# Performance work log

Measured on AMD Instinct MI355X. Metric: run time of the kernel, lower is better.

The kernel has to match this reference:

```python
import jax, jax.numpy as jnp
import numpy as np

B, T, IN = 256, 512, 4      # batch, seq_len, input dim
M, D, NS = 3, 256, 64       # n kaarma models, dictionary size, state dim
H = 128                     # controller (GRU) hidden size
GU, GS = 0.5, 0.5           # gaussian kernel widths (input / state)


def setup_inputs() -> dict:
    key = jax.random.key(0)
    ks = jax.random.split(key, 12)
    s = lambda k, shp, sc: (jax.random.normal(k, shp, dtype=jnp.float32) * sc)
    return {
        "x": s(ks[0], (B, T, IN), 1.0),
        "y": s(ks[1], (B, T), 1.0),
        # MKAARMA: per-model dictionary (inputs U, states S) and coefficients A
        "U": s(ks[2], (M, D, IN), 1.0),
        "S": s(ks[3], (M, D, NS), 0.3),
        "A": s(ks[4], (M, D, NS), 1.0 / np.sqrt(D)),
        # GRU controller (input dim = M + 1 error channel)
        "W_ih": s(ks[5], (M + 1, 3 * H), 1.0 / np.sqrt(M + 1)),
        "W_hh": s(ks[6], (H, 3 * H), 1.0 / np.sqrt(H)),
        "b_ih": s(ks[7], (3 * H,), 0.1),
        "b_hh": s(ks[8], (3 * H,), 0.1),
        # linear_decode: (H-1) -> M gate logits
        "Wd": s(ks[9], (H - 1, M), 1.0 / np.sqrt(H - 1)),
        "bd": s(ks[10], (M,), 0.1),
    }


def _forward(x, y, U, S, A, W_ih, W_hh, b_ih, b_hh, Wd, bd):
    init_gate = jnp.array([[0.3333, 0.3333, 0.3334]], dtype=x.dtype)

    def step(carry, xs):
        s, h, gate_prev, err = carry          # [B,NS], [B,H], [B,M], [B]
        x_t, y_t = xs                         # [B,IN], [B]
        # --- mkaarma: gaussian input*state kernel against dictionary ---
        du = jnp.sum((x_t[:, None, None, :] - U[None]) ** 2, axis=-1)  # [B,M,D]
        ds = jnp.sum((s[:, None, None, :] - S[None]) ** 2, axis=-1)   # [B,M,D]
        K = jnp.exp(-GU * du - GS * ds)                                # [B,M,D]
        new_state = jnp.einsum('bmd,mdn->bmn', K, A)                   # [B,M,NS]
        encoded = jnp.max(K, axis=-1)                                  # [B,M]
        # --- controller: GRU cell on [similarities, error] ---
        inp = jnp.concatenate([encoded, err[:, None]], axis=1)         # [B,M+1]
        gi = inp @ W_ih + b_ih
        gh = h @ W_hh + b_hh
        ir, iz, inn = jnp.split(gi, 3, axis=1)
        hr, hz, hn = jnp.split(gh, 3, axis=1)
        r = jax.nn.sigmoid(ir + hr)
        z = jax.nn.sigmoid(iz + hz)
        n = jnp.tanh(inn + r * hn)
        h_new = (1.0 - z) * n + z * h                                  # [B,H]
        # --- gate decode + theta blend ---
        gate = jax.nn.softmax(h_new[:, :-1] @ Wd + bd, axis=1)          # [B,M]
        theta = jax.nn.sigmoid(h_new[:, -1:])                           # [B,1]
        gate = gate * theta + gate_prev * (1.0 - theta)
        s_new = jnp.einsum('bm,bmn->bn', gate, new_state)               # [B,NS]
        pred = s_new[:, -1]                                             # [B]
        err_new = pred - y_t
        penalty = jnp.sum(gate * (1.0 - gate), axis=1, keepdims=True)   # [B,1]
        return (s_new, h_new, gate, err_new), (pred, penalty)

    carry0 = (
        jnp.zeros((x.shape[0], NS), x.dtype),
        jnp.zeros((x.shape[0], H), x.dtype),
        jnp.tile(init_gate, (x.shape[0], 1)),
        jnp.ones((x.shape[0],), x.dtype),
    )
    xs = (jnp.swapaxes(x, 0, 1), jnp.swapaxes(y, 0, 1))  # time-major
    _, (o, p) = jax.lax.scan(step, carry0, xs)
    return jnp.swapaxes(o, 0, 1), jnp.swapaxes(p, 0, 1)   # [B,T], [B,T,1]


def reference(x, y, U, S, A, W_ih, W_hh, b_ih, b_hh, Wd, bd):
    return _forward(x, y, U, S, A, W_ih, W_hh, b_ih, b_hh, Wd, bd)
```

## Files before the change

kernel.cpp:

```cpp
#include <hip/hip_runtime.h>
#include <math.h>

constexpr int kB  = 256;
constexpr int kT  = 512;
constexpr int kNS = 64;
constexpr int kH  = 128;

constexpr int kWRowsLds = 256;
constexpr int kWPad     = 132;

__device__ __forceinline__ float sigmoidf_(float v) { return 1.0f / (1.0f + __expf(-v)); }
__device__ __forceinline__ float dot4(float4 a, float4 b) {
    return a.x*b.x + a.y*b.y + a.z*b.z + a.w*b.w;
}

extern "C" __global__ void __launch_bounds__(256)
whh_transpose(const float* __restrict__ Whh, float* __restrict__ WhhT) {
    const int o = blockIdx.x * 256 + threadIdx.x;
    const int j = o >> 7, k = o & 127;
    WhhT[o] = Whh[k * 384 + j];
}

extern "C" __global__ void __launch_bounds__(512, 2)
disc_kernel(const float* __restrict__ x,   const float* __restrict__ y,
            const float* __restrict__ U,   const float* __restrict__ S,
            const float* __restrict__ A,   const float* __restrict__ Wih,
            const float* __restrict__ bih, const float* __restrict__ bhh,
            const float* __restrict__ Wd,  const float* __restrict__ bd,
            const float* __restrict__ WhhT,
            float* __restrict__ out_o,  float* __restrict__ out_p)
{
    const int b    = blockIdx.x;
    const int tid  = threadIdx.x;
    const int lane = tid & 63;
    const int wid  = tid >> 6;
    const int hb   = tid & 1;

    __shared__ __align__(16) float sh_K[768];
    __shared__ __align__(16) float sh_part[512];
    __shared__ __align__(16) float sh_part2[512];
    __shared__ __align__(16) float sh_gh[384];
    __shared__ __align__(16) float sh_h[2][kH];
    __shared__ __align__(16) float sh_s[kNS];
    __shared__ __align__(16) float sh_Wih[4 * 384];
    __shared__ __align__(16) float sh_bih[384];
    __shared__ __align__(16) float sh_bhh[384];
    __shared__ float sh_Wd[384];
    __shared__ float sh_bd[4];
    __shared__ float sh_encA[8];
    __shared__ float sh_encB[8];
    __shared__ __align__(16) float sh_xt[4];
    __shared__ float sh_x2, sh_s2, sh_err;
    __shared__ float sh_yt[2];
    __shared__ __align__(16) float sh_W[kWRowsLds * kWPad];

    const float4* S4 = reinterpret_cast<const float4*>(S);
    const float4* U4 = reinterpret_cast<const float4*>(U);

    float4 Sa[16]; float4 Ua; float Ca;
    float4 Sb[8];  float Ub0, Ub1; float Cb;
    {
        float ss = 0.f;
#pragma unroll
        for (int j = 0; j < 16; ++j) { Sa[j] = S4[tid * 16 + j]; ss += dot4(Sa[j], Sa[j]); }
        Ua = U4[tid];
        Ca = -0.5f * (dot4(Ua, Ua) + ss);
    }
    const int pbrow = 512 + (tid >> 1);
    {
        float ss = 0.f;
#pragma unroll
        for (int j = 0; j < 8; ++j) { Sb[j] = S4[pbrow * 16 + hb * 8 + j]; ss += dot4(Sb[j], Sb[j]); }
        Ub0 = U[pbrow * 4 + hb * 2 + 0];
        Ub1 = U[pbrow * 4 + hb * 2 + 1];
        Cb = -0.5f * (Ub0*Ub0 + Ub1*Ub1 + ss);
    }
    float A1[64];
#pragma unroll
    for (int dd = 0; dd < 64; ++dd)
        A1[dd] = A[((wid >> 2) * 256 + (wid & 3) * 64 + dd) * 64 + lane];
    float A2[32];
#pragma unroll
    for (int dd = 0; dd < 32; ++dd)
        A2[dd] = A[(512 + (wid >> 1) * 64 + (wid & 1) * 32 + dd) * 64 + lane];

    float g0 = 0.3333f, g1 = 0.3333f, g2 = 0.3334f;

    for (int i = tid; i < 1536; i += 512) sh_Wih[i] = Wih[i];
    for (int i = tid; i < 384; i += 512) {
        sh_bih[i] = bih[i];
        sh_bhh[i] = bhh[i];
        sh_gh[i]  = bhh[i];
        sh_Wd[i]  = (i < 381) ? Wd[i] : 0.f;
    }
    for (int i4 = tid; i4 < kWRowsLds * 32; i4 += 512) {
        const int r = i4 >> 5, c4 = i4 & 31;
        reinterpret_cast<float4*>(sh_W + r * kWPad)[c4] =
            reinterpret_cast<const float4*>(WhhT)[i4];
    }
    if (tid < 3) sh_bd[tid] = bd[tid];
    if (tid < kNS) sh_s[tid] = 0.f;
    if (tid < kH)  sh_h[0][tid] = 0.f;
    if (tid == 0) {
        sh_err = 1.0f; sh_s2 = 0.f;
        float4 xv = reinterpret_cast<const float4*>(x)[(size_t)b * kT];
        reinterpret_cast<float4*>(sh_xt)[0] = xv;
        sh_x2 = dot4(xv, xv);
        sh_yt[0] = y[(size_t)b * kT];
    }
    __syncthreads();

    for (int t = 0; t < kT; ++t) {
        const int par  = t & 1;
        const int par1 = (t + 1) & 1;

        {
            const float scal = -0.5f * (sh_x2 + sh_s2);
            const float4 xt4 = reinterpret_cast<const float4*>(sh_xt)[0];
            const float4* s4 = reinterpret_cast<const float4*>(sh_s);
            float da0 = 0.f, da1 = 0.f, dblo = 0.f, dbhi = 0.f;
#pragma unroll
            for (int j = 0; j < 8; ++j) {
                const float4 sv0 = s4[j];
                const float4 sv1 = s4[8 + j];
                da0  += dot4(sv0, Sa[j]);
                da1  += dot4(sv1, Sa[8 + j]);
                dblo += dot4(sv0, Sb[j]);
                dbhi += dot4(sv1, Sb[j]);
            }
            const float db = hb ? dbhi : dblo;
            const float kk_a = __expf(scal + Ca + dot4(xt4, Ua) + da0 + da1);
            const float xbp  = hb ? (xt4.z*Ub0 + xt4.w*Ub1) : (xt4.x*Ub0 + xt4.y*Ub1);
            const float ph   = db + Cb + xbp;
            const float po   = __shfl_xor(ph, 1, 64);
            const float kk_b = __expf(scal + ph + po);
            sh_K[tid] = kk_a;
            if (hb == 0) sh_K[512 + (tid >> 1)] = kk_b;
            float mA = kk_a, mB = kk_b;
#pragma unroll
            for (int o = 32; o > 0; o >>= 1) {
                mA = fmaxf(mA, __shfl_xor(mA, o, 64));
                mB = fmaxf(mB, __shfl_xor(mB, o, 64));
            }
            if (lane == 0) { sh_encA[wid] = mA; sh_encB[wid] = mB; }
        }
        __syncthreads();

        {
            const float4* K4 = reinterpret_cast<const float4*>(sh_K + wid * 64);
            float acc = 0.f;
#pragma unroll
            for (int j = 0; j < 16; ++j) {
                const float4 kv = K4[j];
                acc += kv.x*A1[4*j] + kv.y*A1[4*j+1] + kv.z*A1[4*j+2] + kv.w*A1[4*j+3];
            }
            sh_part[tid] = acc;
            const float4* K4b = reinterpret_cast<const float4*>(
                                    sh_K + 512 + (wid >> 1) * 64 + (wid & 1) * 32);
            float accb = 0.f;
#pragma unroll
            for (int j = 0; j < 8; ++j) {
                const float4 kv = K4b[j];
                accb += kv.x*A2[4*j] + kv.y*A2[4*j+1] + kv.z*A2[4*j+2] + kv.w*A2[4*j+3];
            }
            sh_part2[tid] = accb;
        }
        if (tid < 128) {
            const float e0 = fmaxf(fmaxf(sh_encA[0], sh_encA[1]), fmaxf(sh_encA[2], sh_encA[3]));
            const float e1 = fmaxf(fmaxf(sh_encA[4], sh_encA[5]), fmaxf(sh_encA[6], sh_encA[7]));
            const float e2 = fmaxf(fmaxf(fmaxf(sh_encB[0], sh_encB[1]), fmaxf(sh_encB[2], sh_encB[3])),
                                   fmaxf(fmaxf(sh_encB[4], sh_encB[5]), fmaxf(sh_encB[6], sh_encB[7])));
            const float er = sh_err;
            const int j = tid;
            const float gir = sh_bih[j]       + e0*sh_Wih[j]        + e1*sh_Wih[384 + j]
                                              + e2*sh_Wih[768 + j]  + er*sh_Wih[1152 + j];
            const float giz = sh_bih[128 + j] + e0*sh_Wih[128 + j]  + e1*sh_Wih[512 + j]
                                              + e2*sh_Wih[896 + j]  + er*sh_Wih[1280 + j];
            const float gin = sh_bih[256 + j] + e0*sh_Wih[256 + j]  + e1*sh_Wih[640 + j]
                                              + e2*sh_Wih[1024 + j] + er*sh_Wih[1408 + j];
            const float r  = sigmoidf_(gir + sh_gh[j]);
            const float z  = sigmoidf_(giz + sh_gh[128 + j]);
            const float nn = tanhf(gin + r * sh_gh[256 + j]);
            sh_h[par1][j] = (1.f - z) * nn + z * sh_h[par][j];
        }
        __syncthreads();

        if (wid == 0) {
            const float hA = sh_h[par1][lane];
            const float hB = sh_h[par1][64 + lane];
            const float theta = sigmoidf_(sh_h[par1][127]);
            float l0 = hA * sh_Wd[lane*3+0] + hB * sh_Wd[(64+lane)*3+0];
            float l1 = hA * sh_Wd[lane*3+1] + hB * sh_Wd[(64+lane)*3+1];
            float l2 = hA * sh_Wd[lane*3+2] + hB * sh_Wd[(64+lane)*3+2];
#pragma unroll
            for (int o = 32; o > 0; o >>= 1) {
                l0 += __shfl_xor(l0, o, 64);
                l1 += __shfl_xor(l1, o, 64);
                l2 += __shfl_xor(l2, o, 64);
            }
            l0 += sh_bd[0]; l1 += sh_bd[1]; l2 += sh_bd[2];
            const float mx = fmaxf(l0, fmaxf(l1, l2));
            const float x0 = __expf(l0 - mx), x1 = __expf(l1 - mx), x2 = __expf(l2 - mx);
            const float inv = theta / (x0 + x1 + x2);
            const float omt = 1.f - theta;
            g0 = x0*inv + g0*omt;
            g1 = x1*inv + g1*omt;
            g2 = x2*inv + g2*omt;
            const float ns0 = (sh_part[lane]       + sh_part[64 + lane])
                            + (sh_part[128 + lane] + sh_part[192 + lane]);
            const float ns1 = (sh_part[256 + lane] + sh_part[320 + lane])
                            + (sh_part[384 + lane] + sh_part[448 + lane]);
            const float ns2 = ((sh_part2[lane]       + sh_part2[64 + lane])
                            +  (sh_part2[128 + lane] + sh_part2[192 + lane]))
                            + ((sh_part2[256 + lane] + sh_part2[320 + lane])
                            +  (sh_part2[384 + lane] + sh_part2[448 + lane]));
            const float sn = g0*ns0 + g1*ns1 + g2*ns2;
            sh_s[lane] = sn;
            if (lane == 0)
                out_p[(size_t)b * kT + t] = g0*(1.f-g0) + g1*(1.f-g1) + g2*(1.f-g2);
            if (lane == 63) {
                out_o[(size_t)b * kT + t] = sn;
                sh_err = sn - sh_yt[par];
            }
            float ss = sn * sn;
#pragma unroll
            for (int o = 32; o > 0; o >>= 1) ss += __shfl_xor(ss, o, 64);
            if (lane == 0) sh_s2 = ss;
        } else if (wid <= 4) {
            const int u = tid - 64;
            const float4* W4 = reinterpret_cast<const float4*>(sh_W + u * kWPad);
            const float4* h4 = reinterpret_cast<const float4*>(sh_h[par1]);
            float g = sh_bhh[u];
#pragma unroll 8
            for (int k4 = 0; k4 < 32; ++k4)
                g += dot4(h4[k4], W4[k4]);
            sh_gh[u] = g;
        } else if (wid <= 6) {
            const int u = 256 + (tid - 320);
            const float4* W4 = reinterpret_cast<const float4*>(WhhT) + u * 32;
            const float4* h4 = reinterpret_cast<const float4*>(sh_h[par1]);
            float g = sh_bhh[u];
#pragma unroll 8
            for (int k4 = 0; k4 < 32; ++k4)
                g += dot4(h4[k4], W4[k4]);
            sh_gh[u] = g;
        } else {
            if (lane == 0 && (t + 1) < kT) {
                float4 xv = reinterpret_cast<const float4*>(x)[(size_t)b * kT + t + 1];
                reinterpret_cast<float4*>(sh_xt)[0] = xv;
                sh_x2 = dot4(xv, xv);
                sh_yt[par1] = y[(size_t)b * kT + t + 1];
            }
        }
        __syncthreads();
    }
}

extern "C" void kernel_launch(void* const* d_in, const int* in_sizes, int n_in,
                              void* d_out, int out_size, void* d_ws, size_t ws_size,
                              hipStream_t stream)
{
    const float* x   = (const float*)d_in[0];
    const float* y   = (const float*)d_in[1];
    const float* U   = (const float*)d_in[2];
    const float* S   = (const float*)d_in[3];
    const float* A   = (const float*)d_in[4];
    const float* Wih = (const float*)d_in[5];
    const float* Whh = (const float*)d_in[6];
    const float* bih = (const float*)d_in[7];
    const float* bhh = (const float*)d_in[8];
    const float* Wd  = (const float*)d_in[9];
    const float* bd  = (const float*)d_in[10];

    float* WhhT  = (float*)d_ws;
    float* out_o = (float*)d_out;
    float* out_p = out_o + kB * kT;

    hipLaunchKernelGGL(whh_transpose, dim3(192), dim3(256), 0, stream, Whh, WhhT);
    hipLaunchKernelGGL(disc_kernel, dim3(kB), dim3(512), 0, stream,
                       x, y, U, S, A, Wih, bih, bhh, Wd, bd, WhhT, out_o, out_p);
}
```

Before: 2.743 ms.

## Split GRU hidden matvec across phases and use DPP for wave reductions

```diff
diff --git a/kernel.cpp b/kernel.cpp
--- a/kernel.cpp
+++ b/kernel.cpp
@@ -12,6 +12,29 @@
 __device__ __forceinline__ float sigmoidf_(float v) { return 1.0f / (1.0f + __expf(-v)); }
 __device__ __forceinline__ float dot4(float4 a, float4 b) {
     return a.x*b.x + a.y*b.y + a.z*b.z + a.w*b.w;
+}
+
+template <int CTRL>
+__device__ __forceinline__ float dppf(float x) {
+    return __int_as_float(__builtin_amdgcn_mov_dpp(__float_as_int(x), CTRL, 0xf, 0xf, true));
+}
+__device__ __forceinline__ float red_max64(float x) {
+    x = fmaxf(x, dppf<0xB1>(x));
+    x = fmaxf(x, dppf<0x4E>(x));
+    x = fmaxf(x, dppf<0x124>(x));
+    x = fmaxf(x, dppf<0x128>(x));
+    x = fmaxf(x, __shfl_xor(x, 16, 64));
+    x = fmaxf(x, __shfl_xor(x, 32, 64));
+    return x;
+}
+__device__ __forceinline__ float red_sum64(float x) {
+    x += dppf<0xB1>(x);
+    x += dppf<0x4E>(x);
+    x += dppf<0x124>(x);
+    x += dppf<0x128>(x);
+    x += __shfl_xor(x, 16, 64);
+    x += __shfl_xor(x, 32, 64);
+    return x;
 }
 
 extern "C" __global__ void __launch_bounds__(256)
@@ -100,7 +123,7 @@
     }
     if (tid < 3) sh_bd[tid] = bd[tid];
     if (tid < kNS) sh_s[tid] = 0.f;
-    if (tid < kH)  sh_h[0][tid] = 0.f;
+    if (tid < kH)  { sh_h[0][tid] = 0.f; sh_h[1][tid] = 0.f; }
     if (tid == 0) {
         sh_err = 1.0f; sh_s2 = 0.f;
         float4 xv = reinterpret_cast<const float4*>(x)[(size_t)b * kT];
@@ -114,6 +137,25 @@
         const int par  = t & 1;
         const int par1 = (t + 1) & 1;
 
+        if (wid >= 1 && wid <= 4) {
+            const int u = tid - 64;
+            const float4* W4 = reinterpret_cast<const float4*>(sh_W + u * kWPad);
+            const float4* h4 = reinterpret_cast<const float4*>(sh_h[par]);
+            float g = 0.f;
+#pragma unroll 4
+            for (int k4 = 16; k4 < 32; ++k4)
+                g += dot4(h4[k4], W4[k4]);
+            sh_gh[u] += g;
+        } else if (wid == 5 || wid == 6) {
+            const int u = 256 + (tid - 320);
+            const float4* W4 = reinterpret_cast<const float4*>(WhhT) + u * 32;
+            const float4* h4 = reinterpret_cast<const float4*>(sh_h[par]);
+            float g = 0.f;
+#pragma unroll 4
+            for (int k4 = 24; k4 < 32; ++k4)
+                g += dot4(h4[k4], W4[k4]);
+            sh_gh[u] += g;
+        }
         {
             const float scal = -0.5f * (sh_x2 + sh_s2);
             const float4 xt4 = reinterpret_cast<const float4*>(sh_xt)[0];
@@ -132,16 +174,12 @@
             const float kk_a = __expf(scal + Ca + dot4(xt4, Ua) + da0 + da1);
             const float xbp  = hb ? (xt4.z*Ub0 + xt4.w*Ub1) : (xt4.x*Ub0 + xt4.y*Ub1);
             const float ph   = db + Cb + xbp;
-            const float po   = __shfl_xor(ph, 1, 64);
+            const float po   = dppf<0xB1>(ph);
             const float kk_b = __expf(scal + ph + po);
             sh_K[tid] = kk_a;
             if (hb == 0) sh_K[512 + (tid >> 1)] = kk_b;
-            float mA = kk_a, mB = kk_b;
-#pragma unroll
-            for (int o = 32; o > 0; o >>= 1) {
-                mA = fmaxf(mA, __shfl_xor(mA, o, 64));
-                mB = fmaxf(mB, __shfl_xor(mB, o, 64));
-            }
+            const float mA = red_max64(kk_a);
+            const float mB = red_max64(kk_b);
             if (lane == 0) { sh_encA[wid] = mA; sh_encB[wid] = mB; }
         }
         __syncthreads();
@@ -192,12 +230,9 @@
             float l0 = hA * sh_Wd[lane*3+0] + hB * sh_Wd[(64+lane)*3+0];
             float l1 = hA * sh_Wd[lane*3+1] + hB * sh_Wd[(64+lane)*3+1];
             float l2 = hA * sh_Wd[lane*3+2] + hB * sh_Wd[(64+lane)*3+2];
-#pragma unroll
-            for (int o = 32; o > 0; o >>= 1) {
-                l0 += __shfl_xor(l0, o, 64);
-                l1 += __shfl_xor(l1, o, 64);
-                l2 += __shfl_xor(l2, o, 64);
-            }
+            l0 = red_sum64(l0);
+            l1 = red_sum64(l1);
+            l2 = red_sum64(l2);
             l0 += sh_bd[0]; l1 += sh_bd[1]; l2 += sh_bd[2];
             const float mx = fmaxf(l0, fmaxf(l1, l2));
             const float x0 = __expf(l0 - mx), x1 = __expf(l1 - mx), x2 = __expf(l2 - mx);
@@ -222,9 +257,7 @@
                 out_o[(size_t)b * kT + t] = sn;
                 sh_err = sn - sh_yt[par];
             }
-            float ss = sn * sn;
-#pragma unroll
-            for (int o = 32; o > 0; o >>= 1) ss += __shfl_xor(ss, o, 64);
+            const float ss = red_sum64(sn * sn);
             if (lane == 0) sh_s2 = ss;
         } else if (wid <= 4) {
             const int u = tid - 64;
@@ -232,7 +265,7 @@
             const float4* h4 = reinterpret_cast<const float4*>(sh_h[par1]);
             float g = sh_bhh[u];
 #pragma unroll 8
-            for (int k4 = 0; k4 < 32; ++k4)
+            for (int k4 = 0; k4 < 16; ++k4)
                 g += dot4(h4[k4], W4[k4]);
             sh_gh[u] = g;
         } else if (wid <= 6) {
@@ -241,7 +274,7 @@
             const float4* h4 = reinterpret_cast<const float4*>(sh_h[par1]);
             float g = sh_bhh[u];
 #pragma unroll 8
-            for (int k4 = 0; k4 < 32; ++k4)
+            for (int k4 = 0; k4 < 24; ++k4)
                 g += dot4(h4[k4], W4[k4]);
             sh_gh[u] = g;
         } else {
```

Measured after the change: 2.655 ms. 1.03x faster.
